# Kernel tuning notes

Measured on AMD Instinct MI355X. Metric: run time of the kernel, lower is better.

Reference implementation:

```python
import jax, jax.numpy as jnp
import numpy as np


def conv3x3(x, w):
    # x: [B,C,H,W], w: [O,I,3,3], stride 1, pad 1, no bias
    return jax.lax.conv_general_dilated(
        x, w, window_strides=(1, 1), padding=[(1, 1), (1, 1)],
        dimension_numbers=("NCHW", "OIHW", "NCHW"))


def deform_conv2d(x, offset, w):
    """torchvision-style DeformConv2d: k=3, stride=1, pad=1, dilation=1,
    1 offset group, no bias. x:[B,C,H,W], offset:[B,18,H,W] (dy,dx pairs
    per kernel tap, k = kh*3+kw), w:[O,C,3,3]. Zero padding outside."""
    B, C, H, W = x.shape
    K = 9
    dy = offset[:, 0::2]  # [B,9,H,W]
    dx = offset[:, 1::2]
    kh = (jnp.arange(K) // 3 - 1).astype(x.dtype)[None, :, None, None]
    kw = (jnp.arange(K) % 3 - 1).astype(x.dtype)[None, :, None, None]
    hh = jnp.arange(H, dtype=x.dtype)[None, None, :, None]
    ww = jnp.arange(W, dtype=x.dtype)[None, None, None, :]
    py = hh + kh + dy  # sampling y coord, [B,9,H,W]
    px = ww + kw + dx
    y0 = jnp.floor(py)
    x0 = jnp.floor(px)
    wy = py - y0
    wx = px - x0
    x_hwc = jnp.transpose(x, (0, 2, 3, 1))  # [B,H,W,C]
    b_idx = jnp.arange(B)[:, None, None, None]

    def gather(yi, xi):
        valid = (yi >= 0) & (yi <= H - 1) & (xi >= 0) & (xi <= W - 1)
        yc = jnp.clip(yi, 0, H - 1).astype(jnp.int32)
        xc = jnp.clip(xi, 0, W - 1).astype(jnp.int32)
        v = x_hwc[b_idx, yc, xc]  # [B,9,H,W,C]
        return v * valid[..., None].astype(x.dtype)

    v00 = gather(y0, x0)
    v01 = gather(y0, x0 + 1)
    v10 = gather(y0 + 1, x0)
    v11 = gather(y0 + 1, x0 + 1)
    wy = wy[..., None]
    wx = wx[..., None]
    sampled = (v00 * (1 - wy) * (1 - wx) + v01 * (1 - wy) * wx
               + v10 * wy * (1 - wx) + v11 * wy * wx)  # [B,9,H,W,C]
    wk = w.reshape(w.shape[0], w.shape[1], K)  # [O,C,9]
    return jnp.einsum("bkhwc,ock->bohw", sampled, wk)


def setup_inputs() -> dict:
    key = jax.random.key(0)
    ks = jax.random.split(key, 6)
    B, C, H, W = 2, 128, 128, 128
    s = 0.05  # small init so learned offsets stay in a realistic range
    return {
        "input_features": jax.random.normal(ks[0], (B, C, H, W), jnp.float32),
        "reference_features": jax.random.normal(ks[1], (B, C, H, W), jnp.float32),
        "w_est1": jax.random.normal(ks[2], (C, 2 * C, 3, 3), jnp.float32) * s,
        "w_est2": jax.random.normal(ks[3], (C, C, 3, 3), jnp.float32) * s,
        "w_off": jax.random.normal(ks[4], (18, C, 3, 3), jnp.float32) * s,
        "w_def": jax.random.normal(ks[5], (C, C, 3, 3), jnp.float32) * s,
    }


def reference(input_features, reference_features, w_est1, w_est2, w_off, w_def):
    # concat input+reference features along channel dim
    feat = jnp.concatenate([input_features, reference_features], axis=1)  # [B,2C,H,W]
    # dynamic offset estimator: 2-layer 3x3 conv stack 2C->C->C with ReLU
    est = jax.nn.relu(conv3x3(feat, w_est1))
    est = jax.nn.relu(conv3x3(est, w_est2))
    # offset head: C -> 2*9 offsets per pixel
    offset = conv3x3(est, w_off)  # [B,18,H,W]
    # deformable conv over the reference features
    return deform_conv2d(reference_features, offset, w_def)
```

## Files before the change

### kernel.cpp

```cpp
#include <hip/hip_runtime.h>

typedef _Float16 f16;
typedef __attribute__((ext_vector_type(8))) _Float16 f16x8;
typedef __attribute__((ext_vector_type(4))) float f32x4;
typedef __attribute__((ext_vector_type(4))) int i32x4;


__device__ __forceinline__ void g2l16(const void* g, void* l) {
  __builtin_amdgcn_global_load_lds((const __attribute__((address_space(1))) void*)g,
                                   (__attribute__((address_space(3))) void*)l, 16, 0, 0);
}

__device__ __forceinline__ void pack_conv(const float* __restrict__ src, f16* __restrict__ dst,
                                          long idx, int C) {
  int ci3 = idx & 7;
  int g = (idx >> 3) & 3;
  long t = idx >> 5;
  int o = (int)(t & 63); t >>= 6;
  int kx = (int)(t % 3); t /= 3;
  int nb = (int)(t & 1); t >>= 1;
  int nkc = C >> 5;
  int cc = (int)(t % nkc);
  int ky = (int)(t / nkc);
  int og = nb * 64 + o;
  int c = (cc << 5) + ((g ^ ((o >> 1) & 3)) << 3) + ci3;
  dst[idx] = (f16)src[(((size_t)og * C + c) * 3 + ky) * 3 + kx];
}

__device__ __forceinline__ void halo_zero(f16* __restrict__ buf, long e) {
  int c = (int)(e & 127);
  long t = e >> 7;
  int b = (int)(t / 516);
  int p = (int)(t % 516);
  int y, x;
  if (p < 130)      { y = 0;   x = p; }
  else if (p < 260) { y = 129; x = p - 130; }
  else if (p < 388) { x = 0;   y = p - 259; }
  else              { x = 129; y = p - 387; }
  buf[((size_t)(b * 130 + y) * 130 + x) * 128 + c] = (f16)0.f;
}

__global__ __launch_bounds__(256) void init_k(const float* __restrict__ x, const float* __restrict__ ref,
                                              const float* __restrict__ w1, const float* __restrict__ w2,
                                              const float* __restrict__ woff, const float* __restrict__ wdef,
                                              f16* __restrict__ W1p, f16* __restrict__ W2p,
                                              f16* __restrict__ Woffp, f16* __restrict__ Wdefp,
                                              f16* __restrict__ xP, f16* __restrict__ refP,
                                              f16* __restrict__ est1, f16* __restrict__ est2) {
  __shared__ __align__(16) f16 T[64][40];
  int tid = threadIdx.x;
  if (blockIdx.x < 4096) {
    int bi = blockIdx.x;
    int row = bi & 255, wseg = (bi >> 8) & 1, chunk = bi >> 9;
    int b = row >> 7, h = row & 127;
    int w0 = wseg * 64;
    const float* src = (chunk < 4) ? x : ref;
    f16* dstp = (chunk < 4) ? xP : refP;
    int c0 = (chunk & 3) * 32;
#pragma unroll
    for (int i = 0; i < 2; ++i) {
      int idx = tid + i * 256;
      int c = idx >> 4, g = idx & 15;
      const float4 v = *(const float4*)(src + (((size_t)(b * 128 + c0 + c)) * 128 + h) * 128 + w0 + g * 4);
      T[g * 4 + 0][c] = (f16)v.x;
      T[g * 4 + 1][c] = (f16)v.y;
      T[g * 4 + 2][c] = (f16)v.z;
      T[g * 4 + 3][c] = (f16)v.w;
    }
    __syncthreads();
    int w = tid >> 2, g = tid & 3;
    f16x8 o = *(const f16x8*)&T[w][g * 8];
    *(f16x8*)(dstp + ((size_t)(b * 130 + h + 1) * 130 + w0 + w + 1) * 128 + c0 + g * 8) = o;
    return;
  }
  long idx = (long)(blockIdx.x - 4096) * 256 + tid;
  if (idx < 294912) { pack_conv(w1, W1p, idx, 256); return; }
  idx -= 294912;
  if (idx < 147456) { pack_conv(w2, W2p, idx, 128); return; }
  idx -= 147456;
  if (idx < 36864) {
    int ci3 = (int)(idx & 7);
    int g = (int)((idx >> 3) & 3);
    int o = (int)((idx >> 5) & 31);
    int t2 = (int)(idx >> 10);
    int kx = t2 % 3; t2 /= 3;
    int cc = t2 & 3, ky = t2 >> 2;
    int c = (cc << 5) + ((g ^ ((o >> 1) & 3)) << 3) + ci3;
    Woffp[idx] = (o < 18) ? (f16)woff[(((size_t)o * 128 + c) * 3 + ky) * 3 + kx] : (f16)0.f;
    return;
  }
  idx -= 36864;
  if (idx < 147456) {
    int j = (int)(idx & 7);
    int ln = (int)((idx >> 3) & 63);
    int ofr = (int)((idx >> 9) & 7);
    int cc = (int)((idx >> 12) & 3);
    int t = (int)(idx >> 14);
    int o = ofr * 16 + (ln & 15);
    int c = cc * 32 + (ln >> 4) * 8 + j;
    Wdefp[idx] = (f16)wdef[(((size_t)o * 128 + c) * 3 + t / 3) * 3 + t % 3];
    return;
  }
  idx -= 147456;
  if (idx < 132096) { halo_zero(xP, idx); return; }
  idx -= 132096;
  if (idx < 132096) { halo_zero(refP, idx); return; }
  idx -= 132096;
  if (idx < 132096) { halo_zero(est1, idx); return; }
  idx -= 132096;
  if (idx < 132096) halo_zero(est2, idx);
}

template <int NKC>
__global__ __launch_bounds__(256, 2) void conv_k(const f16* __restrict__ src0,
                                                 const f16* __restrict__ src1,
                                                 const f16* __restrict__ Wp,
                                                 f16* __restrict__ dst) {
  constexpr int S = 3 * NKC;
  const int j = blockIdx.x;
  const int xcd = j & 7, ji = j >> 3;
  const int row = xcd * 32 + (ji & 31);
  const int nb = ji >> 5;
  const int b = row >> 7, h = row & 127;
  __shared__ __align__(16) f16 As[2][130][32];
  __shared__ __align__(16) f16 Bs[2][3][64][32];
  const int tid = threadIdx.x;
  const int lane = tid & 63, wave = tid >> 6;
  const int l16 = lane & 15, quad = lane >> 4;
  const int wmB = wave * 32;
  f32x4 acc[2][4] = {};

  i32x4 ra0, ra1, ra2, rb0, rb1, rb2;

  auto stage_load = [&](int s) {
    int ky = s / NKC, cc = s % NKC;
    const f16* sp = (NKC == 8 && cc >= 4) ? src1 : src0;
    int c0 = (NKC == 8 ? (cc & 3) : cc) * 32;
    const f16* abase = sp + ((size_t)(b * 130 + h + ky) * 130) * 128 + c0;
    {
      int ch = tid;
      int xx = ch >> 2, g = ch & 3;
      ra0 = *(const i32x4*)(abase + (size_t)xx * 128 + ((g ^ ((xx >> 1) & 3)) << 3));
    }
    {
      int ch = 256 + tid;
      int xx = ch >> 2, g = ch & 3;
      ra1 = *(const i32x4*)(abase + (size_t)xx * 128 + ((g ^ ((xx >> 1) & 3)) << 3));
    }
    if (tid < 8) {
      int ch = 512 + tid;
      int xx = ch >> 2, g = ch & 3;
      ra2 = *(const i32x4*)(abase + (size_t)xx * 128 + ((g ^ ((xx >> 1) & 3)) << 3));
    }
    const f16* bbase = Wp + (size_t)((ky * NKC + cc) * 2 + nb) * (3 * 64 * 32);
    rb0 = *(const i32x4*)(bbase + (size_t)tid * 8);
    rb1 = *(const i32x4*)(bbase + (size_t)(256 + tid) * 8);
    rb2 = *(const i32x4*)(bbase + (size_t)(512 + tid) * 8);
  };
  auto stage_write = [&](int buf) {
    *(i32x4*)((char*)&As[buf][0][0] + tid * 16) = ra0;
    *(i32x4*)((char*)&As[buf][0][0] + (256 + tid) * 16) = ra1;
    if (tid < 8)
      *(i32x4*)((char*)&As[buf][0][0] + (512 + tid) * 16) = ra2;
    *(i32x4*)((char*)&Bs[buf][0][0][0] + tid * 16) = rb0;
    *(i32x4*)((char*)&Bs[buf][0][0][0] + (256 + tid) * 16) = rb1;
    *(i32x4*)((char*)&Bs[buf][0][0][0] + (512 + tid) * 16) = rb2;
  };

  stage_load(0);
  stage_write(0);
  stage_load(1);
  __syncthreads();
  for (int s = 0; s < S; ++s) {
    const int buf = s & 1;
#pragma unroll
    for (int kx = 0; kx < 3; ++kx) {
      f16x8 bf[4];
#pragma unroll
      for (int j2 = 0; j2 < 4; ++j2) {
        int o = j2 * 16 + l16;
        bf[j2] = *(const f16x8*)&Bs[buf][kx][o][(quad ^ ((o >> 1) & 3)) << 3];
      }
#pragma unroll
      for (int i = 0; i < 2; ++i) {
        int xx = wmB + i * 16 + l16 + kx;
        f16x8 a = *(const f16x8*)&As[buf][xx][(quad ^ ((xx >> 1) & 3)) << 3];
#pragma unroll
        for (int j2 = 0; j2 < 4; ++j2)
          acc[i][j2] = __builtin_amdgcn_mfma_f32_16x16x32_f16(a, bf[j2], acc[i][j2], 0, 0, 0);
      }
    }
    __syncthreads();
    if (s + 1 < S) stage_write((s + 1) & 1);
    if (s + 2 < S) stage_load(s + 2);
    __syncthreads();
  }
#pragma unroll
  for (int i = 0; i < 2; ++i)
#pragma unroll
    for (int j2 = 0; j2 < 4; ++j2) {
      int o = nb * 64 + j2 * 16 + l16;
#pragma unroll
      for (int rr = 0; rr < 4; ++rr) {
        int m = wmB + i * 16 + quad * 4 + rr;
        float v = fmaxf(acc[i][j2][rr], 0.f);
        dst[((size_t)(b * 130 + h + 1) * 130 + m + 1) * 128 + o] = (f16)v;
      }
    }
}

__global__ __launch_bounds__(256, 2) void conv_off_k(const f16* __restrict__ src,
                                                     const f16* __restrict__ Wp,
                                                     float* __restrict__ dst) {
  const int j = blockIdx.x;
  const int row = (j & 7) * 32 + (j >> 3);
  const int b = row >> 7, h = row & 127;
  __shared__ __align__(16) f16 As[2][130][32];
  __shared__ __align__(16) f16 Bs[2][3][32][32];
  const int tid = threadIdx.x;
  const int lane = tid & 63, wave = tid >> 6;
  const int l16 = lane & 15, quad = lane >> 4;
  const int wmB = wave * 32;
  f32x4 acc[2][2] = {};

  i32x4 ra0, ra1, ra2, rb0, rb1;

  auto stage_load = [&](int s) {
    int ky = s >> 2, cc = s & 3;
    const f16* abase = src + ((size_t)(b * 130 + h + ky) * 130) * 128 + cc * 32;
    {
      int ch = tid;
      int xx = ch >> 2, g = ch & 3;
      ra0 = *(const i32x4*)(abase + (size_t)xx * 128 + ((g ^ ((xx >> 1) & 3)) << 3));
    }
    {
      int ch = 256 + tid;
      int xx = ch >> 2, g = ch & 3;
      ra1 = *(const i32x4*)(abase + (size_t)xx * 128 + ((g ^ ((xx >> 1) & 3)) << 3));
    }
    if (tid < 8) {
      int ch = 512 + tid;
      int xx = ch >> 2, g = ch & 3;
      ra2 = *(const i32x4*)(abase + (size_t)xx * 128 + ((g ^ ((xx >> 1) & 3)) << 3));
    }
    const f16* bbase = Wp + (size_t)(ky * 4 + cc) * (3 * 32 * 32);
    rb0 = *(const i32x4*)(bbase + (size_t)tid * 8);
    if (tid < 128) rb1 = *(const i32x4*)(bbase + (size_t)(256 + tid) * 8);
  };
  auto stage_write = [&](int buf) {
    *(i32x4*)((char*)&As[buf][0][0] + tid * 16) = ra0;
    *(i32x4*)((char*)&As[buf][0][0] + (256 + tid) * 16) = ra1;
    if (tid < 8)
      *(i32x4*)((char*)&As[buf][0][0] + (512 + tid) * 16) = ra2;
    *(i32x4*)((char*)&Bs[buf][0][0][0] + tid * 16) = rb0;
    if (tid < 128)
      *(i32x4*)((char*)&Bs[buf][0][0][0] + (256 + tid) * 16) = rb1;
  };

  stage_load(0);
  stage_write(0);
  stage_load(1);
  __syncthreads();
  for (int s = 0; s < 12; ++s) {
    const int buf = s & 1;
#pragma unroll
    for (int kx = 0; kx < 3; ++kx) {
      f16x8 bf[2];
#pragma unroll
      for (int j2 = 0; j2 < 2; ++j2) {
        int o = j2 * 16 + l16;
        bf[j2] = *(const f16x8*)&Bs[buf][kx][o][(quad ^ ((o >> 1) & 3)) << 3];
      }
#pragma unroll
      for (int i = 0; i < 2; ++i) {
        int xx = wmB + i * 16 + l16 + kx;
        f16x8 a = *(const f16x8*)&As[buf][xx][(quad ^ ((xx >> 1) & 3)) << 3];
#pragma unroll
        for (int j2 = 0; j2 < 2; ++j2)
          acc[i][j2] = __builtin_amdgcn_mfma_f32_16x16x32_f16(a, bf[j2], acc[i][j2], 0, 0, 0);
      }
    }
    __syncthreads();
    if (s + 1 < 12) stage_write((s + 1) & 1);
    if (s + 2 < 12) stage_load(s + 2);
    __syncthreads();
  }
#pragma unroll
  for (int i = 0; i < 2; ++i)
#pragma unroll
    for (int j2 = 0; j2 < 2; ++j2)
#pragma unroll
      for (int rr = 0; rr < 4; ++rr) {
        int m = wmB + i * 16 + quad * 4 + rr;
        int o = j2 * 16 + l16;
        dst[((size_t)row * 128 + m) * 32 + o] = acc[i][j2][rr];
      }
}

__global__ __launch_bounds__(256, 2) void deform_k(const f16* __restrict__ refP,
                                                   const float* __restrict__ offb,
                                                   const f16* __restrict__ Wdefp,
                                                   float* __restrict__ out) {
  const int j = blockIdx.x;
  const int xcd = j & 7, ji = j >> 3;
  const int row = xcd * 32 + (ji & 31);
  const int tile = ji >> 5;
  const int b = row >> 7, h = row & 127;
  __shared__ __align__(16) f16 Ss[2][64][128];
  __shared__ int4 meta[9][64];
  const int tid = threadIdx.x;
  const int lane = tid & 63, wave = tid >> 6;
  const int l16 = lane & 15, quad = lane >> 4;

  for (int e = tid; e < 576; e += 256) {
    int t = e >> 6, p = e & 63;
    int wg = tile * 64 + p;
    const float2 d = *(const float2*)(offb + ((size_t)row * 128 + wg) * 32 + 2 * t);
    float py = (float)(h + t / 3 - 1) + d.x;
    float px = (float)(wg + t % 3 - 1) + d.y;
    float fy = floorf(py), fx = floorf(px);
    meta[t][p] = make_int4((int)fy, (int)fx, __float_as_int(py - fy), __float_as_int(px - fx));
  }

  const int sp_p = tid >> 2, sp_cg = tid & 3;
  f16x8 v00[4], v01[4], v10[4], v11[4];
  f16 h00, h01, h10, h11;

  auto sample_issue = [&](int t) {
    int4 mt = meta[t][sp_p];
    int yp = mt.x + 1, xp = mt.y + 1;
    float wy = __int_as_float(mt.z), wx = __int_as_float(mt.w);
    bool y0v = (unsigned)yp < 130u, y1v = (unsigned)(yp + 1) < 130u;
    bool x0v = (unsigned)xp < 130u, x1v = (unsigned)(xp + 1) < 130u;
    int cy0 = y0v ? yp : 0, cy1 = y1v ? yp + 1 : 0;
    int cx0 = x0v ? xp : 0, cx1 = x1v ? xp + 1 : 0;
    float u0 = (1.f - wy) * (y0v ? 1.f : 0.f), u1 = wy * (y1v ? 1.f : 0.f);
    float s0 = (1.f - wx) * (x0v ? 1.f : 0.f), s1 = wx * (x1v ? 1.f : 0.f);
    h00 = (f16)(u0 * s0); h01 = (f16)(u0 * s1);
    h10 = (f16)(u1 * s0); h11 = (f16)(u1 * s1);
    const size_t bb = (size_t)b * 130;
    const f16* p00 = refP + ((bb + cy0) * 130 + cx0) * 128 + sp_cg * 32;
    const f16* p01 = refP + ((bb + cy0) * 130 + cx1) * 128 + sp_cg * 32;
    const f16* p10 = refP + ((bb + cy1) * 130 + cx0) * 128 + sp_cg * 32;
    const f16* p11 = refP + ((bb + cy1) * 130 + cx1) * 128 + sp_cg * 32;
#pragma unroll
    for (int q = 0; q < 4; ++q) {
      v00[q] = *(const f16x8*)(p00 + q * 8);
      v01[q] = *(const f16x8*)(p01 + q * 8);
      v10[q] = *(const f16x8*)(p10 + q * 8);
      v11[q] = *(const f16x8*)(p11 + q * 8);
    }
  };
  auto sample_finish = [&](int buf) {
#pragma unroll
    for (int q = 0; q < 4; ++q) {
      f16x8 rb = v00[q] * h00 + v01[q] * h01 + v10[q] * h10 + v11[q] * h11;
      int c = sp_cg * 4 + q;
      *(f16x8*)&Ss[buf][sp_p][(c ^ (sp_p & 7)) << 3] = rb;
    }
  };

  f32x4 acc[2][4] = {};
  __syncthreads();
  sample_issue(0);
  sample_finish(0);
  __syncthreads();
  for (int t = 0; t < 9; ++t) {
    f16x8 af[4][2];
#pragma unroll
    for (int cc = 0; cc < 4; ++cc)
#pragma unroll
      for (int i = 0; i < 2; ++i)
        af[cc][i] = *(const f16x8*)(Wdefp +
            ((((size_t)t * 4 + cc) * 8 + wave * 2 + i) * 64 + lane) * 8);
    if (t < 8) sample_issue(t + 1);
    const int buf = t & 1;
#pragma unroll
    for (int cc = 0; cc < 4; ++cc) {
      f16x8 bf[4];
#pragma unroll
      for (int j2 = 0; j2 < 4; ++j2) {
        int p = j2 * 16 + l16;
        bf[j2] = *(const f16x8*)&Ss[buf][p][((cc * 4 + quad) ^ (p & 7)) << 3];
      }
#pragma unroll
      for (int i = 0; i < 2; ++i)
#pragma unroll
        for (int j2 = 0; j2 < 4; ++j2)
          acc[i][j2] = __builtin_amdgcn_mfma_f32_16x16x32_f16(af[cc][i], bf[j2], acc[i][j2], 0, 0, 0);
    }
    if (t < 8) sample_finish((t + 1) & 1);
    __syncthreads();
  }
#pragma unroll
  for (int i = 0; i < 2; ++i)
#pragma unroll
    for (int rr = 0; rr < 4; ++rr) {
      int o = wave * 32 + i * 16 + quad * 4 + rr;
#pragma unroll
      for (int j2 = 0; j2 < 4; ++j2) {
        int wg = tile * 64 + j2 * 16 + l16;
        out[((size_t)(b * 128 + o) * 128 + h) * 128 + wg] = acc[i][j2][rr];
      }
    }
}

extern "C" void kernel_launch(void* const* d_in, const int* in_sizes, int n_in,
                              void* d_out, int out_size, void* d_ws, size_t ws_size,
                              hipStream_t stream) {
  const float* x = (const float*)d_in[0];
  const float* ref = (const float*)d_in[1];
  const float* w1 = (const float*)d_in[2];
  const float* w2 = (const float*)d_in[3];
  const float* woff = (const float*)d_in[4];
  const float* wdef = (const float*)d_in[5];
  float* out = (float*)d_out;
  char* ws = (char*)d_ws;
  f16* xP = (f16*)(ws + 0);
  f16* refP = (f16*)(ws + 8652800);
  f16* est1 = (f16*)(ws + 17305600);
  f16* est2 = (f16*)(ws + 25958400);
  float* offb = (float*)(ws + 34611200);
  f16* W1p = (f16*)(ws + 38805504);
  f16* W2p = (f16*)(ws + 39395328);
  f16* Woffp = (f16*)(ws + 39690240);
  f16* Wdefp = (f16*)(ws + 39763968);

  init_k<<<dim3(8608), 256, 0, stream>>>(x, ref, w1, w2, woff, wdef,
                                         W1p, W2p, Woffp, Wdefp, xP, refP, est1, est2);
  conv_k<8><<<dim3(512), 256, 0, stream>>>(xP, refP, W1p, est1);
  conv_k<4><<<dim3(512), 256, 0, stream>>>(est1, est1, W2p, est2);
  conv_off_k<<<dim3(256), 256, 0, stream>>>(est2, Woffp, offb);
  deform_k<<<dim3(512), 256, 0, stream>>>(refP, offb, Wdefp, out);
}
```

Baseline: 161.3 us.

## Fuse all stages into one persistent kernel with software grid barriers

Replaces the five separate launches (init, two convs, offset conv, deformable conv) with one persistent 512-block kernel. Stages are separated by an atomic-counter grid barrier, and each stage reuses a shared LDS buffer. The aim is to remove launch gaps and inter-kernel drain and fill. In exchange the init phase is grid-strided over fewer blocks, the barrier relies on all 512 blocks being co-resident (2 per CU on 256 CUs), and it adds a memset plus atomic spin traffic.

```diff
diff --git a/kernel.cpp b/kernel.cpp
--- a/kernel.cpp
+++ b/kernel.cpp
@@ -6,9 +6,24 @@
 typedef __attribute__((ext_vector_type(4))) int i32x4;
 
 
-__device__ __forceinline__ void g2l16(const void* g, void* l) {
-  __builtin_amdgcn_global_load_lds((const __attribute__((address_space(1))) void*)g,
-                                   (__attribute__((address_space(3))) void*)l, 16, 0, 0);
+__device__ __forceinline__ void grid_barrier(unsigned* bar, unsigned nb) {
+  __syncthreads();
+  if (threadIdx.x == 0) {
+    unsigned* cnt = bar;
+    unsigned* gen = bar + 32;
+    unsigned g = __hip_atomic_load(gen, __ATOMIC_RELAXED, __HIP_MEMORY_SCOPE_AGENT);
+    __threadfence();
+    unsigned arrived = __hip_atomic_fetch_add(cnt, 1u, __ATOMIC_ACQ_REL, __HIP_MEMORY_SCOPE_AGENT);
+    if (arrived == nb - 1) {
+      __hip_atomic_store(cnt, 0u, __ATOMIC_RELAXED, __HIP_MEMORY_SCOPE_AGENT);
+      __hip_atomic_fetch_add(gen, 1u, __ATOMIC_RELEASE, __HIP_MEMORY_SCOPE_AGENT);
+    } else {
+      while (__hip_atomic_load(gen, __ATOMIC_ACQUIRE, __HIP_MEMORY_SCOPE_AGENT) == g)
+        __builtin_amdgcn_s_sleep(2);
+    }
+    __threadfence();
+  }
+  __syncthreads();
 }
 
 __device__ __forceinline__ void pack_conv(const float* __restrict__ src, f16* __restrict__ dst,
@@ -40,90 +55,84 @@
   buf[((size_t)(b * 130 + y) * 130 + x) * 128 + c] = (f16)0.f;
 }
 
-__global__ __launch_bounds__(256) void init_k(const float* __restrict__ x, const float* __restrict__ ref,
-                                              const float* __restrict__ w1, const float* __restrict__ w2,
-                                              const float* __restrict__ woff, const float* __restrict__ wdef,
-                                              f16* __restrict__ W1p, f16* __restrict__ W2p,
-                                              f16* __restrict__ Woffp, f16* __restrict__ Wdefp,
-                                              f16* __restrict__ xP, f16* __restrict__ refP,
-                                              f16* __restrict__ est1, f16* __restrict__ est2) {
-  __shared__ __align__(16) f16 T[64][40];
-  int tid = threadIdx.x;
-  if (blockIdx.x < 4096) {
-    int bi = blockIdx.x;
-    int row = bi & 255, wseg = (bi >> 8) & 1, chunk = bi >> 9;
-    int b = row >> 7, h = row & 127;
-    int w0 = wseg * 64;
-    const float* src = (chunk < 4) ? x : ref;
-    f16* dstp = (chunk < 4) ? xP : refP;
-    int c0 = (chunk & 3) * 32;
-#pragma unroll
-    for (int i = 0; i < 2; ++i) {
-      int idx = tid + i * 256;
-      int c = idx >> 4, g = idx & 15;
-      const float4 v = *(const float4*)(src + (((size_t)(b * 128 + c0 + c)) * 128 + h) * 128 + w0 + g * 4);
-      T[g * 4 + 0][c] = (f16)v.x;
-      T[g * 4 + 1][c] = (f16)v.y;
-      T[g * 4 + 2][c] = (f16)v.z;
-      T[g * 4 + 3][c] = (f16)v.w;
-    }
-    __syncthreads();
-    int w = tid >> 2, g = tid & 3;
-    f16x8 o = *(const f16x8*)&T[w][g * 8];
-    *(f16x8*)(dstp + ((size_t)(b * 130 + h + 1) * 130 + w0 + w + 1) * 128 + c0 + g * 8) = o;
-    return;
-  }
-  long idx = (long)(blockIdx.x - 4096) * 256 + tid;
-  if (idx < 294912) { pack_conv(w1, W1p, idx, 256); return; }
-  idx -= 294912;
-  if (idx < 147456) { pack_conv(w2, W2p, idx, 128); return; }
-  idx -= 147456;
-  if (idx < 36864) {
-    int ci3 = (int)(idx & 7);
-    int g = (int)((idx >> 3) & 3);
-    int o = (int)((idx >> 5) & 31);
-    int t2 = (int)(idx >> 10);
-    int kx = t2 % 3; t2 /= 3;
-    int cc = t2 & 3, ky = t2 >> 2;
-    int c = (cc << 5) + ((g ^ ((o >> 1) & 3)) << 3) + ci3;
-    Woffp[idx] = (o < 18) ? (f16)woff[(((size_t)o * 128 + c) * 3 + ky) * 3 + kx] : (f16)0.f;
-    return;
-  }
-  idx -= 36864;
-  if (idx < 147456) {
-    int j = (int)(idx & 7);
-    int ln = (int)((idx >> 3) & 63);
-    int ofr = (int)((idx >> 9) & 7);
-    int cc = (int)((idx >> 12) & 3);
-    int t = (int)(idx >> 14);
-    int o = ofr * 16 + (ln & 15);
-    int c = cc * 32 + (ln >> 4) * 8 + j;
-    Wdefp[idx] = (f16)wdef[(((size_t)o * 128 + c) * 3 + t / 3) * 3 + t % 3];
-    return;
-  }
-  idx -= 147456;
-  if (idx < 132096) { halo_zero(xP, idx); return; }
-  idx -= 132096;
-  if (idx < 132096) { halo_zero(refP, idx); return; }
-  idx -= 132096;
-  if (idx < 132096) { halo_zero(est1, idx); return; }
-  idx -= 132096;
-  if (idx < 132096) halo_zero(est2, idx);
+__device__ __forceinline__ void init_phase(char* smem,
+    const float* __restrict__ x, const float* __restrict__ ref,
+    const float* __restrict__ w1, const float* __restrict__ w2,
+    const float* __restrict__ woff, const float* __restrict__ wdef,
+    f16* __restrict__ W1p, f16* __restrict__ W2p,
+    f16* __restrict__ Woffp, f16* __restrict__ Wdefp,
+    f16* __restrict__ xP, f16* __restrict__ refP,
+    f16* __restrict__ est1, f16* __restrict__ est2) {
+  f16 (*T)[40] = (f16(*)[40])smem;
+  const int tid = threadIdx.x;
+  for (int vb = blockIdx.x; vb < 8608; vb += 512) {
+    if (vb < 4096) {
+      int row = vb & 255, wseg = (vb >> 8) & 1, chunk = vb >> 9;
+      int b = row >> 7, h = row & 127;
+      int w0 = wseg * 64;
+      const float* src = (chunk < 4) ? x : ref;
+      f16* dstp = (chunk < 4) ? xP : refP;
+      int c0 = (chunk & 3) * 32;
+#pragma unroll
+      for (int i = 0; i < 2; ++i) {
+        int idx = tid + i * 256;
+        int c = idx >> 4, g = idx & 15;
+        const float4 v = *(const float4*)(src + (((size_t)(b * 128 + c0 + c)) * 128 + h) * 128 + w0 + g * 4);
+        T[g * 4 + 0][c] = (f16)v.x;
+        T[g * 4 + 1][c] = (f16)v.y;
+        T[g * 4 + 2][c] = (f16)v.z;
+        T[g * 4 + 3][c] = (f16)v.w;
+      }
+      __syncthreads();
+      int w = tid >> 2, g = tid & 3;
+      f16x8 o = *(const f16x8*)&T[w][g * 8];
+      *(f16x8*)(dstp + ((size_t)(b * 130 + h + 1) * 130 + w0 + w + 1) * 128 + c0 + g * 8) = o;
+      __syncthreads();
+    } else {
+      long idx = (long)(vb - 4096) * 256 + tid;
+      if (idx < 294912) pack_conv(w1, W1p, idx, 256);
+      else if ((idx -= 294912) < 147456) pack_conv(w2, W2p, idx, 128);
+      else if ((idx -= 147456) < 36864) {
+        int ci3 = (int)(idx & 7);
+        int g = (int)((idx >> 3) & 3);
+        int o = (int)((idx >> 5) & 31);
+        int t2 = (int)(idx >> 10);
+        int kx = t2 % 3; t2 /= 3;
+        int cc = t2 & 3, ky = t2 >> 2;
+        int c = (cc << 5) + ((g ^ ((o >> 1) & 3)) << 3) + ci3;
+        Woffp[idx] = (o < 18) ? (f16)woff[(((size_t)o * 128 + c) * 3 + ky) * 3 + kx] : (f16)0.f;
+      } else if ((idx -= 36864) < 147456) {
+        int jj = (int)(idx & 7);
+        int ln = (int)((idx >> 3) & 63);
+        int ofr = (int)((idx >> 9) & 7);
+        int cc = (int)((idx >> 12) & 3);
+        int t = (int)(idx >> 14);
+        int o = ofr * 16 + (ln & 15);
+        int c = cc * 32 + (ln >> 4) * 8 + jj;
+        Wdefp[idx] = (f16)wdef[(((size_t)o * 128 + c) * 3 + t / 3) * 3 + t % 3];
+      }
+      else if ((idx -= 147456) < 132096) halo_zero(xP, idx);
+      else if ((idx -= 132096) < 132096) halo_zero(refP, idx);
+      else if ((idx -= 132096) < 132096) halo_zero(est1, idx);
+      else if ((idx -= 132096) < 132096) halo_zero(est2, idx);
+    }
+  }
 }
 
 template <int NKC>
-__global__ __launch_bounds__(256, 2) void conv_k(const f16* __restrict__ src0,
-                                                 const f16* __restrict__ src1,
-                                                 const f16* __restrict__ Wp,
-                                                 f16* __restrict__ dst) {
+__device__ __forceinline__ void conv_phase(char* smem,
+                                           const f16* __restrict__ src0,
+                                           const f16* __restrict__ src1,
+                                           const f16* __restrict__ Wp,
+                                           f16* __restrict__ dst) {
   constexpr int S = 3 * NKC;
   const int j = blockIdx.x;
   const int xcd = j & 7, ji = j >> 3;
   const int row = xcd * 32 + (ji & 31);
   const int nb = ji >> 5;
   const int b = row >> 7, h = row & 127;
-  __shared__ __align__(16) f16 As[2][130][32];
-  __shared__ __align__(16) f16 Bs[2][3][64][32];
+  f16 (*As)[130][32] = (f16(*)[130][32])smem;
+  f16 (*Bs)[3][64][32] = (f16(*)[3][64][32])(smem + 16640);
   const int tid = threadIdx.x;
   const int lane = tid & 63, wave = tid >> 6;
   const int l16 = lane & 15, quad = lane >> 4;
@@ -209,14 +218,15 @@
     }
 }
 
-__global__ __launch_bounds__(256, 2) void conv_off_k(const f16* __restrict__ src,
-                                                     const f16* __restrict__ Wp,
-                                                     float* __restrict__ dst) {
+__device__ __forceinline__ void conv_off_phase(char* smem,
+                                               const f16* __restrict__ src,
+                                               const f16* __restrict__ Wp,
+                                               float* __restrict__ dst) {
   const int j = blockIdx.x;
   const int row = (j & 7) * 32 + (j >> 3);
   const int b = row >> 7, h = row & 127;
-  __shared__ __align__(16) f16 As[2][130][32];
-  __shared__ __align__(16) f16 Bs[2][3][32][32];
+  f16 (*As)[130][32] = (f16(*)[130][32])smem;
+  f16 (*Bs)[3][32][32] = (f16(*)[3][32][32])(smem + 16640);
   const int tid = threadIdx.x;
   const int lane = tid & 63, wave = tid >> 6;
   const int l16 = lane & 15, quad = lane >> 4;
@@ -297,17 +307,18 @@
       }
 }
 
-__global__ __launch_bounds__(256, 2) void deform_k(const f16* __restrict__ refP,
-                                                   const float* __restrict__ offb,
-                                                   const f16* __restrict__ Wdefp,
-                                                   float* __restrict__ out) {
+__device__ __forceinline__ void deform_phase(char* smem,
+                                             const f16* __restrict__ refP,
+                                             const float* __restrict__ offb,
+                                             const f16* __restrict__ Wdefp,
+                                             float* __restrict__ out) {
   const int j = blockIdx.x;
   const int xcd = j & 7, ji = j >> 3;
   const int row = xcd * 32 + (ji & 31);
   const int tile = ji >> 5;
   const int b = row >> 7, h = row & 127;
-  __shared__ __align__(16) f16 Ss[2][64][128];
-  __shared__ int4 meta[9][64];
+  f16 (*Ss)[64][128] = (f16(*)[64][128])smem;
+  int4 (*meta)[64] = (int4(*)[64])(smem + 32768);
   const int tid = threadIdx.x;
   const int lane = tid & 63, wave = tid >> 6;
   const int l16 = lane & 15, quad = lane >> 4;
@@ -403,6 +414,29 @@
         out[((size_t)(b * 128 + o) * 128 + h) * 128 + wg] = acc[i][j2][rr];
       }
     }
+}
+
+__global__ __launch_bounds__(256, 2) void mega_k(
+    const float* __restrict__ x, const float* __restrict__ ref,
+    const float* __restrict__ w1, const float* __restrict__ w2,
+    const float* __restrict__ woff, const float* __restrict__ wdef,
+    f16* __restrict__ W1p, f16* __restrict__ W2p,
+    f16* __restrict__ Woffp, f16* __restrict__ Wdefp,
+    f16* __restrict__ xP, f16* __restrict__ refP,
+    f16* __restrict__ est1, f16* __restrict__ est2,
+    float* __restrict__ offb, float* __restrict__ out,
+    unsigned* __restrict__ bar) {
+  __shared__ __align__(16) char smem[42496];
+
+  init_phase(smem, x, ref, w1, w2, woff, wdef, W1p, W2p, Woffp, Wdefp, xP, refP, est1, est2);
+  grid_barrier(bar, 512);
+  conv_phase<8>(smem, xP, refP, W1p, est1);
+  grid_barrier(bar, 512);
+  conv_phase<4>(smem, est1, est1, W2p, est2);
+  grid_barrier(bar, 512);
+  if (blockIdx.x < 256) conv_off_phase(smem, est2, Woffp, offb);
+  grid_barrier(bar, 512);
+  deform_phase(smem, refP, offb, Wdefp, out);
 }
 
 extern "C" void kernel_launch(void* const* d_in, const int* in_sizes, int n_in,
@@ -425,11 +459,10 @@
   f16* W2p = (f16*)(ws + 39395328);
   f16* Woffp = (f16*)(ws + 39690240);
   f16* Wdefp = (f16*)(ws + 39763968);
-
-  init_k<<<dim3(8608), 256, 0, stream>>>(x, ref, w1, w2, woff, wdef,
-                                         W1p, W2p, Woffp, Wdefp, xP, refP, est1, est2);
-  conv_k<8><<<dim3(512), 256, 0, stream>>>(xP, refP, W1p, est1);
-  conv_k<4><<<dim3(512), 256, 0, stream>>>(est1, est1, W2p, est2);
-  conv_off_k<<<dim3(256), 256, 0, stream>>>(est2, Woffp, offb);
-  deform_k<<<dim3(512), 256, 0, stream>>>(refP, offb, Wdefp, out);
-}
+  unsigned* bar = (unsigned*)(ws + 40058880);
+
+  hipMemsetAsync(bar, 0, 256, stream);
+  mega_k<<<dim3(512), dim3(256), 0, stream>>>(x, ref, w1, w2, woff, wdef,
+                                              W1p, W2p, Woffp, Wdefp,
+                                              xP, refP, est1, est2, offb, out, bar);
+}
```

Measured after the change: 408.7 us. 153% more time.
